# Optimization experiments

Hardware: AMD Instinct MI355X
Metric: run time of the kernel (lower is better)

Reference implementation:

```python
import jax, jax.numpy as jnp
import numpy as np

NUM_HEADS = 8
NUM_POINTS = 4


def setup_inputs() -> dict:
    key = jax.random.key(0)
    ks = jax.random.split(key, 10)
    B, H, W, D = 8, 64, 64, 256
    N = H * W
    nh, P = NUM_HEADS, NUM_POINTS

    def xavier(k, shape):
        fan_in, fan_out = shape[0], shape[1]
        lim = float(np.sqrt(6.0 / (fan_in + fan_out)))
        return jax.random.uniform(k, shape, jnp.float32, -lim, lim)

    x = jax.random.normal(ks[0], (B, N, D), jnp.float32)
    qkv_w = xavier(ks[1], (D, 3 * D))
    qkv_b = jnp.zeros((3 * D,), jnp.float32)
    # offset network is zero-init in the module; use small random weights so the
    # deformable sampling is actually exercised (offsets nonzero).
    off_w = jax.random.normal(ks[2], (D, nh * P * 2), jnp.float32) * 0.01
    off_b = jnp.zeros((nh * P * 2,), jnp.float32)
    attw_w = xavier(ks[3], (D, nh * P))
    attw_b = jnp.zeros((nh * P,), jnp.float32)
    proj_w = xavier(ks[4], (D, D))
    proj_b = jnp.zeros((D,), jnp.float32)
    return {
        "x": x, "qkv_w": qkv_w, "qkv_b": qkv_b,
        "off_w": off_w, "off_b": off_b,
        "attw_w": attw_w, "attw_b": attw_b,
        "proj_w": proj_w, "proj_b": proj_b,
        "H": 64, "W": 64,
    }


def _deformable_forward(x, qkv_w, qkv_b, off_w, off_b, attw_w, attw_b, proj_w, proj_b, H, W):
    B, N, D = x.shape
    nh, P = NUM_HEADS, NUM_POINTS
    hd = D // nh

    qkv = x @ qkv_w + qkv_b                      # [B,N,3D] (q,k computed but unused, as in the original)
    v = qkv[..., 2 * D:].reshape(B, N, nh, hd)   # [B,N,nh,hd]

    offsets = jnp.tanh((x @ off_w + off_b).reshape(B, N, nh, P, 2)) * 2.0

    ys, xs = jnp.meshgrid(jnp.arange(H, dtype=x.dtype), jnp.arange(W, dtype=x.dtype), indexing="ij")
    ref = jnp.stack([xs, ys], axis=-1).reshape(N, 2)          # [N,2] (x,y) pixel coords
    loc = ref[None, :, None, None, :] + offsets               # [B,N,nh,P,2] pixel coords
    # (module normalizes to [-1,1] then grid_sample align_corners=True un-normalizes
    #  back to exactly these pixel coordinates, so we sample at `loc` directly)

    # value as flat spatial map per head: [B,nh,hd,N], n = y*W + x
    vf = v.transpose(0, 2, 3, 1).reshape(B, nh, hd, N)

    gx, gy = loc[..., 0], loc[..., 1]
    x0 = jnp.floor(gx); y0 = jnp.floor(gy)
    x1 = x0 + 1.0;      y1 = y0 + 1.0
    wx1 = gx - x0; wx0 = 1.0 - wx1
    wy1 = gy - y0; wy0 = 1.0 - wy1

    def corner(xi, yi, w):
        # bilinear corner with zeros padding: zero weight if corner out of bounds
        valid = (xi >= 0) & (xi < W) & (yi >= 0) & (yi < H)
        idx = (jnp.clip(yi, 0, H - 1) * W + jnp.clip(xi, 0, W - 1)).astype(jnp.int32)
        idx2 = idx.transpose(0, 2, 1, 3).reshape(B, nh, N * P)          # [B,nh,N*P]
        g = jnp.take_along_axis(vf, idx2[:, :, None, :], axis=3)        # [B,nh,hd,N*P]
        w2 = (w * valid.astype(x.dtype)).transpose(0, 2, 1, 3).reshape(B, nh, 1, N * P)
        return g * w2

    sampled = (corner(x0, y0, wx0 * wy0) + corner(x1, y0, wx1 * wy0)
               + corner(x0, y1, wx0 * wy1) + corner(x1, y1, wx1 * wy1))
    sampled = sampled.reshape(B, nh, hd, N, P)

    attn = jax.nn.softmax((x @ attw_w + attw_b).reshape(B, N, nh, P), axis=-1)
    out = jnp.einsum("bhcnp,bnhp->bnhc", sampled, attn).reshape(B, N, D)
    return out @ proj_w + proj_b


def reference(x, qkv_w, qkv_b, off_w, off_b, attw_w, attw_b, proj_w, proj_b, H, W):
    return _deformable_forward(x, qkv_w, qkv_b, off_w, off_b, attw_w, attw_b, proj_w, proj_b, H, W)
```

## Files before the change

kernel.cpp:

```cpp
#include <hip/hip_runtime.h>
#include <hip/hip_bf16.h>
#include <cmath>

#define NN 4096
typedef __attribute__((ext_vector_type(8))) short short8;
typedef __attribute__((ext_vector_type(4))) float f32x4;

__device__ __forceinline__ float bf2f(unsigned short u) {
  union { unsigned int i; float f; } c; c.i = ((unsigned int)u) << 16; return c.f;
}

__global__ __launch_bounds__(256) void cvt_w(
    const float* __restrict__ qkv_w, const float* __restrict__ off_w,
    const float* __restrict__ attw_w, const float* __restrict__ proj_w,
    __hip_bfloat16* __restrict__ wcatT, __hip_bfloat16* __restrict__ pjT)
{
  const int t = threadIdx.x;
  if (blockIdx.x < 256) {
    int k = blockIdx.x;
    wcatT[t * 256 + k] = __float2bfloat16(qkv_w[k * 768 + 512 + t]);
    if (t < 128) {
      int c2 = 256 + t;
      float v = 0.f;
      if (c2 < 320)      v = off_w[k * 64 + (c2 - 256)];
      else if (c2 < 352) v = attw_w[k * 32 + (c2 - 320)];
      wcatT[c2 * 256 + k] = __float2bfloat16(v);
    }
  } else {
    int k = blockIdx.x - 256;
    pjT[t * 256 + k] = __float2bfloat16(proj_w[k * 256 + t]);
  }
}

__global__ __launch_bounds__(512) void gemm_voff(
    const float* __restrict__ x,
    const __hip_bfloat16* __restrict__ wcatT,
    const float* __restrict__ vbias,
    const float* __restrict__ off_b, const float* __restrict__ attw_b,
    __hip_bfloat16* __restrict__ vb,
    unsigned int* __restrict__ table)
{
  __shared__ float smemf[12800];
  short* As = (short*)smemf;
  short* Bs = As + 128 * 40;
  float (*L)[100] = (float(*)[100])smemf;

  const int t = threadIdx.x;
  const int m0 = blockIdx.x * 128;
  const int wave = t >> 6, lane = t & 63, q = lane >> 4, ln = lane & 15;
  const int wm = (wave & 1) * 64, wn = (wave >> 1) * 96;

  f32x4 acc[4][6] = {};

  const int arow = t >> 2, aseg = t & 3;
  const float* apg = x + (size_t)(m0 + arow) * 256 + aseg * 8;

  for (int k0 = 0; k0 < 256; k0 += 32) {
    float4 f0 = *(const float4*)(apg + k0);
    float4 f1 = *(const float4*)(apg + k0 + 4);
    alignas(16) __hip_bfloat16 cv[8] = {
      __float2bfloat16(f0.x), __float2bfloat16(f0.y), __float2bfloat16(f0.z), __float2bfloat16(f0.w),
      __float2bfloat16(f1.x), __float2bfloat16(f1.y), __float2bfloat16(f1.z), __float2bfloat16(f1.w)};
    *(int4*)&As[arow * 40 + aseg * 8] = *(int4*)cv;
#pragma unroll
    for (int i = 0; i < 3; ++i) {
      int u = t + i * 512;
      int brow = u >> 2, bseg = u & 3;
      *(int4*)&Bs[brow * 40 + bseg * 8] =
          *(const int4*)&wcatT[(size_t)brow * 256 + k0 + bseg * 8];
    }
    __syncthreads();
    short8 a[4], b[6];
#pragma unroll
    for (int i = 0; i < 4; ++i) a[i] = *(const short8*)&As[(wm + i * 16 + ln) * 40 + q * 8];
#pragma unroll
    for (int j = 0; j < 6; ++j) b[j] = *(const short8*)&Bs[(wn + j * 16 + ln) * 40 + q * 8];
#pragma unroll
    for (int i = 0; i < 4; ++i)
#pragma unroll
      for (int j = 0; j < 6; ++j)
        acc[i][j] = __builtin_amdgcn_mfma_f32_16x16x32_bf16(a[i], b[j], acc[i][j], 0, 0, 0);
    __syncthreads();
  }

#pragma unroll
  for (int j = 0; j < 6; ++j) {
    int col = wn + j * 16 + ln;
    if (col < 256) {
      float bv = vbias[col];
#pragma unroll
      for (int i = 0; i < 4; ++i) {
        int rowb = m0 + wm + i * 16 + q * 4;
#pragma unroll
        for (int r = 0; r < 4; ++r)
          vb[(size_t)(rowb + r) * 256 + col] = __float2bfloat16(acc[i][j][r] + bv);
      }
    } else if (col < 352) {
      int lc = col - 256;
      float bv = (lc < 64) ? off_b[lc] : attw_b[lc - 64];
#pragma unroll
      for (int i = 0; i < 4; ++i)
#pragma unroll
        for (int r = 0; r < 4; ++r)
          L[wm + i * 16 + q * 4 + r][lc] = acc[i][j][r] + bv;
    }
  }
  __syncthreads();

#pragma unroll
  for (int it = 0; it < 2; ++it) {
    int pl = t + it * 512;
    int rr = pl >> 3, h = pl & 7;
    int row = m0 + rr;
    int nl = row & (NN - 1);
    float refx = (float)(nl & 63);
    float refy = (float)(nl >> 6);

    float a0 = L[rr][64 + h * 4 + 0], a1 = L[rr][64 + h * 4 + 1];
    float a2 = L[rr][64 + h * 4 + 2], a3 = L[rr][64 + h * 4 + 3];
    float mx = fmaxf(fmaxf(a0, a1), fmaxf(a2, a3));
    float e0 = expf(a0 - mx), e1 = expf(a1 - mx), e2 = expf(a2 - mx), e3 = expf(a3 - mx);
    float inv = 1.f / (e0 + e1 + e2 + e3);
    float at[4] = {e0 * inv, e1 * inv, e2 * inv, e3 * inv};

    alignas(16) unsigned short idxs[16];
    alignas(16) _Float16 wsv[16];
#pragma unroll
    for (int p = 0; p < 4; ++p) {
      float gx = refx + 2.f * tanhf(L[rr][h * 8 + p * 2 + 0]);
      float gy = refy + 2.f * tanhf(L[rr][h * 8 + p * 2 + 1]);
      float x0f = floorf(gx), y0f = floorf(gy);
      int x0 = (int)x0f, y0 = (int)y0f;
      int x1 = x0 + 1,   y1 = y0 + 1;
      float wx1 = gx - x0f, wx0 = 1.f - wx1;
      float wy1 = gy - y0f, wy0 = 1.f - wy1;
      int cx0 = min(max(x0, 0), 63), cx1 = min(max(x1, 0), 63);
      int cy0 = min(max(y0, 0), 63), cy1 = min(max(y1, 0), 63);
      float vx0 = (x0 >= 0 && x0 <= 63) ? 1.f : 0.f;
      float vx1 = (x1 >= 0 && x1 <= 63) ? 1.f : 0.f;
      float vy0 = (y0 >= 0 && y0 <= 63) ? 1.f : 0.f;
      float vy1 = (y1 >= 0 && y1 <= 63) ? 1.f : 0.f;
      float ap = at[p];
      idxs[p * 4 + 0] = (unsigned short)(cy0 * 64 + cx0);
      idxs[p * 4 + 1] = (unsigned short)(cy0 * 64 + cx1);
      idxs[p * 4 + 2] = (unsigned short)(cy1 * 64 + cx0);
      idxs[p * 4 + 3] = (unsigned short)(cy1 * 64 + cx1);
      wsv[p * 4 + 0] = (_Float16)(ap * wx0 * wy0 * vx0 * vy0);
      wsv[p * 4 + 1] = (_Float16)(ap * wx1 * wy0 * vx1 * vy0);
      wsv[p * 4 + 2] = (_Float16)(ap * wx0 * wy1 * vx0 * vy1);
      wsv[p * 4 + 3] = (_Float16)(ap * wx1 * wy1 * vx1 * vy1);
    }
    uint4* dst = (uint4*)(table + ((size_t)row * 8 + h) * 16);
    dst[0] = *(uint4*)&idxs[0];
    dst[1] = *(uint4*)&idxs[8];
    dst[2] = *(uint4*)&wsv[0];
    dst[3] = *(uint4*)&wsv[8];
  }
}

__global__ __launch_bounds__(256) void sample_kernel(
    const __hip_bfloat16* __restrict__ v,
    const unsigned int* __restrict__ table,
    __hip_bfloat16* __restrict__ y)
{
  __shared__ uint4 Tab[256];
  const int t = threadIdx.x;
  const int p0 = blockIdx.x * 64;
  Tab[t] = *(const uint4*)(table + (size_t)p0 * 16 + t * 4);
  __syncthreads();

  const int g = t & 3, p = t >> 2;
  const int pg = p0 + p;
  const int h = pg & 7;
  const int row = pg >> 3;
  const int b = row >> 12;
  const unsigned short* ip = (const unsigned short*)&Tab[p * 4];
  const _Float16* wp = (const _Float16*)((const char*)&Tab[p * 4] + 32);
  const char* vbase = (const char*)(v + (size_t)b * NN * 256 + h * 32 + g * 8);

  float acc[8] = {};
#pragma unroll
  for (int j = 0; j < 16; ++j) {
    float w = (float)wp[j];
    int idx = ip[j];
    int4 pk = *(const int4*)(vbase + (size_t)idx * 512);
    const unsigned short* u = (const unsigned short*)&pk;
#pragma unroll
    for (int c = 0; c < 8; ++c) acc[c] += w * bf2f(u[c]);
  }
  alignas(16) __hip_bfloat16 o[8];
#pragma unroll
  for (int c = 0; c < 8; ++c) o[c] = __float2bfloat16(acc[c]);
  *(int4*)((char*)y + ((size_t)row * 256 + h * 32 + g * 8) * 2) = *(int4*)o;
}

__global__ __launch_bounds__(256) void gemm_proj(
    const short* __restrict__ A, const short* __restrict__ BT,
    const float* __restrict__ bias, float* __restrict__ out)
{
  __shared__ short As[128 * 40];
  __shared__ short Bs[128 * 40];
  const int t = threadIdx.x;
  const int m0 = blockIdx.y * 128, n0 = blockIdx.x * 128;
  const int wave = t >> 6, lane = t & 63, q = lane >> 4, ln = lane & 15;
  const int wm = (wave & 1) * 64, wn = (wave >> 1) * 64;

  f32x4 acc[4][4] = {};

  for (int k0 = 0; k0 < 256; k0 += 32) {
#pragma unroll
    for (int u = 0; u < 2; ++u) {
      int c = t + u * 256;
      int row = c >> 2, kq = c & 3;
      *(int4*)&As[row * 40 + kq * 8] =
          *(const int4*)&A[(size_t)(m0 + row) * 256 + k0 + kq * 8];
      *(int4*)&Bs[row * 40 + kq * 8] =
          *(const int4*)&BT[(size_t)(n0 + row) * 256 + k0 + kq * 8];
    }
    __syncthreads();
    short8 a[4], b[4];
#pragma unroll
    for (int i = 0; i < 4; ++i) a[i] = *(const short8*)&As[(wm + i * 16 + ln) * 40 + q * 8];
#pragma unroll
    for (int j = 0; j < 4; ++j) b[j] = *(const short8*)&Bs[(wn + j * 16 + ln) * 40 + q * 8];
#pragma unroll
    for (int i = 0; i < 4; ++i)
#pragma unroll
      for (int j = 0; j < 4; ++j)
        acc[i][j] = __builtin_amdgcn_mfma_f32_16x16x32_bf16(a[i], b[j], acc[i][j], 0, 0, 0);
    __syncthreads();
  }

#pragma unroll
  for (int j = 0; j < 4; ++j) {
    int col = n0 + wn + j * 16 + ln;
    float bv = bias[col];
#pragma unroll
    for (int i = 0; i < 4; ++i) {
      int rowb = m0 + wm + i * 16 + q * 4;
#pragma unroll
      for (int r = 0; r < 4; ++r)
        out[(size_t)(rowb + r) * 256 + col] = acc[i][j][r] + bv;
    }
  }
}

extern "C" void kernel_launch(void* const* d_in, const int* in_sizes, int n_in,
                              void* d_out, int out_size, void* d_ws, size_t ws_size,
                              hipStream_t stream) {
  const float* x      = (const float*)d_in[0];
  const float* qkv_w  = (const float*)d_in[1];
  const float* qkv_b  = (const float*)d_in[2];
  const float* off_w  = (const float*)d_in[3];
  const float* off_b  = (const float*)d_in[4];
  const float* attw_w = (const float*)d_in[5];
  const float* attw_b = (const float*)d_in[6];
  const float* proj_w = (const float*)d_in[7];
  const float* proj_b = (const float*)d_in[8];
  float* out = (float*)d_out;

  char* ws = (char*)d_ws;
  __hip_bfloat16* vb    = (__hip_bfloat16*)(ws);
  __hip_bfloat16* yb    = (__hip_bfloat16*)(ws + 16777216);
  unsigned int*   table = (unsigned int*)  (ws + 33554432);
  __hip_bfloat16* wcatT = (__hip_bfloat16*)(ws + 50331648);
  __hip_bfloat16* pjT   = (__hip_bfloat16*)(ws + 50528256);

  cvt_w<<<512, 256, 0, stream>>>(qkv_w, off_w, attw_w, proj_w, wcatT, pjT);
  gemm_voff<<<256, 512, 0, stream>>>(x, wcatT, qkv_b + 512, off_b, attw_b, vb, table);
  sample_kernel<<<4096, 256, 0, stream>>>(vb, table, yb);
  dim3 g2(2, 256);
  gemm_proj<<<g2, 256, 0, stream>>>((const short*)yb, (const short*)pjT, proj_b, out);
}
```

Measured before the change: 152.6 us.

## Fuse deformable sampling into projection GEMM and shrink voff GEMM tiles

The bilinear sampling kernel and the output projection GEMM become one kernel. Each 64-row block gathers its sampled values into an LDS tile and multiplies it by the projection weights there. This removes the intermediate y buffer write/read and one launch. The value/offset GEMM also moves to 64-row tiles with 256 threads, giving 512 blocks instead of 256. The costs are that the projection weights are reloaded for every 64-row block, and the larger LDS footprint may reduce occupancy while the gather phase runs.

After: 169.8 us. 1.11x slower.

```diff
diff --git a/kernel.cpp b/kernel.cpp
--- a/kernel.cpp
+++ b/kernel.cpp
@@ -32,7 +32,7 @@
   }
 }
 
-__global__ __launch_bounds__(512) void gemm_voff(
+__global__ __launch_bounds__(256) void gemm_voff(
     const float* __restrict__ x,
     const __hip_bfloat16* __restrict__ wcatT,
     const float* __restrict__ vbias,
@@ -40,15 +40,15 @@
     __hip_bfloat16* __restrict__ vb,
     unsigned int* __restrict__ table)
 {
-  __shared__ float smemf[12800];
+  __shared__ float smemf[8960];
   short* As = (short*)smemf;
-  short* Bs = As + 128 * 40;
+  short* Bs = As + 64 * 40;
   float (*L)[100] = (float(*)[100])smemf;
 
   const int t = threadIdx.x;
-  const int m0 = blockIdx.x * 128;
+  const int m0 = blockIdx.x * 64;
   const int wave = t >> 6, lane = t & 63, q = lane >> 4, ln = lane & 15;
-  const int wm = (wave & 1) * 64, wn = (wave >> 1) * 96;
+  const int wn = wave * 96;
 
   f32x4 acc[4][6] = {};
 
@@ -63,8 +63,8 @@
       __float2bfloat16(f1.x), __float2bfloat16(f1.y), __float2bfloat16(f1.z), __float2bfloat16(f1.w)};
     *(int4*)&As[arow * 40 + aseg * 8] = *(int4*)cv;
 #pragma unroll
-    for (int i = 0; i < 3; ++i) {
-      int u = t + i * 512;
+    for (int i = 0; i < 6; ++i) {
+      int u = t + i * 256;
       int brow = u >> 2, bseg = u & 3;
       *(int4*)&Bs[brow * 40 + bseg * 8] =
           *(const int4*)&wcatT[(size_t)brow * 256 + k0 + bseg * 8];
@@ -72,7 +72,7 @@
     __syncthreads();
     short8 a[4], b[6];
 #pragma unroll
-    for (int i = 0; i < 4; ++i) a[i] = *(const short8*)&As[(wm + i * 16 + ln) * 40 + q * 8];
+    for (int i = 0; i < 4; ++i) a[i] = *(const short8*)&As[(i * 16 + ln) * 40 + q * 8];
 #pragma unroll
     for (int j = 0; j < 6; ++j) b[j] = *(const short8*)&Bs[(wn + j * 16 + ln) * 40 + q * 8];
 #pragma unroll
@@ -90,7 +90,7 @@
       float bv = vbias[col];
 #pragma unroll
       for (int i = 0; i < 4; ++i) {
-        int rowb = m0 + wm + i * 16 + q * 4;
+        int rowb = m0 + i * 16 + q * 4;
 #pragma unroll
         for (int r = 0; r < 4; ++r)
           vb[(size_t)(rowb + r) * 256 + col] = __float2bfloat16(acc[i][j][r] + bv);
@@ -102,14 +102,14 @@
       for (int i = 0; i < 4; ++i)
 #pragma unroll
         for (int r = 0; r < 4; ++r)
-          L[wm + i * 16 + q * 4 + r][lc] = acc[i][j][r] + bv;
+          L[i * 16 + q * 4 + r][lc] = acc[i][j][r] + bv;
     }
   }
   __syncthreads();
 
 #pragma unroll
   for (int it = 0; it < 2; ++it) {
-    int pl = t + it * 512;
+    int pl = t + it * 256;
     int rr = pl >> 3, h = pl & 7;
     int row = m0 + rr;
     int nl = row & (NN - 1);
@@ -158,86 +158,80 @@
   }
 }
 
-__global__ __launch_bounds__(256) void sample_kernel(
-    const __hip_bfloat16* __restrict__ v,
+__global__ __launch_bounds__(256) void gemm_sproj(
+    const __hip_bfloat16* __restrict__ vb,
     const unsigned int* __restrict__ table,
-    __hip_bfloat16* __restrict__ y)
+    const __hip_bfloat16* __restrict__ pjT,
+    const float* __restrict__ bias,
+    float* __restrict__ out)
 {
-  __shared__ uint4 Tab[256];
+  __shared__ short ytile[64 * 264];
+  __shared__ short Bs[256 * 40];
   const int t = threadIdx.x;
-  const int p0 = blockIdx.x * 64;
-  Tab[t] = *(const uint4*)(table + (size_t)p0 * 16 + t * 4);
+  const int m0 = blockIdx.x * 64;
+  const int wave = t >> 6, lane = t & 63, q = lane >> 4, ln = lane & 15;
+  const int wn = wave * 64;
+  const int b = m0 >> 12;
+
+#pragma unroll
+  for (int i = 0; i < 8; ++i) {
+    int tau = t + i * 256;
+    int r = tau >> 5, h = (tau >> 2) & 7, g = tau & 3;
+    int row = m0 + r;
+    const uint4* tp = (const uint4*)(table + ((size_t)row * 8 + h) * 16);
+    uint4 e0 = tp[0], e1 = tp[1];
+    uint4 e2 = tp[2], e3 = tp[3];
+    const unsigned int iw[8] = {e0.x, e0.y, e0.z, e0.w, e1.x, e1.y, e1.z, e1.w};
+    const unsigned int ww[8] = {e2.x, e2.y, e2.z, e2.w, e3.x, e3.y, e3.z, e3.w};
+    const char* vbase = (const char*)(vb + ((size_t)b * NN * 256) + h * 32 + g * 8);
+    float accg[8] = {};
+#pragma unroll
+    for (int j = 0; j < 16; ++j) {
+      unsigned int idx = (iw[j >> 1] >> ((j & 1) * 16)) & 0xffffu;
+      union { unsigned int u; _Float16 h2[2]; } wu; wu.u = ww[j >> 1];
+      float w = (float)wu.h2[j & 1];
+      int4 pk = *(const int4*)(vbase + (size_t)idx * 512);
+      const unsigned short* uu = (const unsigned short*)&pk;
+#pragma unroll
+      for (int c = 0; c < 8; ++c) accg[c] += w * bf2f(uu[c]);
+    }
+    alignas(16) __hip_bfloat16 o[8];
+#pragma unroll
+    for (int c = 0; c < 8; ++c) o[c] = __float2bfloat16(accg[c]);
+    *(int4*)&ytile[r * 264 + h * 32 + g * 8] = *(int4*)o;
+  }
   __syncthreads();
 
-  const int g = t & 3, p = t >> 2;
-  const int pg = p0 + p;
-  const int h = pg & 7;
-  const int row = pg >> 3;
-  const int b = row >> 12;
-  const unsigned short* ip = (const unsigned short*)&Tab[p * 4];
-  const _Float16* wp = (const _Float16*)((const char*)&Tab[p * 4] + 32);
-  const char* vbase = (const char*)(v + (size_t)b * NN * 256 + h * 32 + g * 8);
-
-  float acc[8] = {};
-#pragma unroll
-  for (int j = 0; j < 16; ++j) {
-    float w = (float)wp[j];
-    int idx = ip[j];
-    int4 pk = *(const int4*)(vbase + (size_t)idx * 512);
-    const unsigned short* u = (const unsigned short*)&pk;
-#pragma unroll
-    for (int c = 0; c < 8; ++c) acc[c] += w * bf2f(u[c]);
-  }
-  alignas(16) __hip_bfloat16 o[8];
-#pragma unroll
-  for (int c = 0; c < 8; ++c) o[c] = __float2bfloat16(acc[c]);
-  *(int4*)((char*)y + ((size_t)row * 256 + h * 32 + g * 8) * 2) = *(int4*)o;
-}
-
-__global__ __launch_bounds__(256) void gemm_proj(
-    const short* __restrict__ A, const short* __restrict__ BT,
-    const float* __restrict__ bias, float* __restrict__ out)
-{
-  __shared__ short As[128 * 40];
-  __shared__ short Bs[128 * 40];
-  const int t = threadIdx.x;
-  const int m0 = blockIdx.y * 128, n0 = blockIdx.x * 128;
-  const int wave = t >> 6, lane = t & 63, q = lane >> 4, ln = lane & 15;
-  const int wm = (wave & 1) * 64, wn = (wave >> 1) * 64;
-
   f32x4 acc[4][4] = {};
-
   for (int k0 = 0; k0 < 256; k0 += 32) {
 #pragma unroll
-    for (int u = 0; u < 2; ++u) {
-      int c = t + u * 256;
-      int row = c >> 2, kq = c & 3;
-      *(int4*)&As[row * 40 + kq * 8] =
-          *(const int4*)&A[(size_t)(m0 + row) * 256 + k0 + kq * 8];
-      *(int4*)&Bs[row * 40 + kq * 8] =
-          *(const int4*)&BT[(size_t)(n0 + row) * 256 + k0 + kq * 8];
-    }
-    __syncthreads();
-    short8 a[4], b[4];
-#pragma unroll
-    for (int i = 0; i < 4; ++i) a[i] = *(const short8*)&As[(wm + i * 16 + ln) * 40 + q * 8];
-#pragma unroll
-    for (int j = 0; j < 4; ++j) b[j] = *(const short8*)&Bs[(wn + j * 16 + ln) * 40 + q * 8];
+    for (int i = 0; i < 4; ++i) {
+      int u = t + i * 256;
+      int brow = u >> 2, bseg = u & 3;
+      *(int4*)&Bs[brow * 40 + bseg * 8] =
+          *(const int4*)&pjT[(size_t)brow * 256 + k0 + bseg * 8];
+    }
+    __syncthreads();
+    short8 a[4], bfr[4];
+#pragma unroll
+    for (int i = 0; i < 4; ++i) a[i] = *(const short8*)&ytile[(i * 16 + ln) * 264 + k0 + q * 8];
+#pragma unroll
+    for (int j = 0; j < 4; ++j) bfr[j] = *(const short8*)&Bs[(wn + j * 16 + ln) * 40 + q * 8];
 #pragma unroll
     for (int i = 0; i < 4; ++i)
 #pragma unroll
       for (int j = 0; j < 4; ++j)
-        acc[i][j] = __builtin_amdgcn_mfma_f32_16x16x32_bf16(a[i], b[j], acc[i][j], 0, 0, 0);
+        acc[i][j] = __builtin_amdgcn_mfma_f32_16x16x32_bf16(a[i], bfr[j], acc[i][j], 0, 0, 0);
     __syncthreads();
   }
 
 #pragma unroll
   for (int j = 0; j < 4; ++j) {
-    int col = n0 + wn + j * 16 + ln;
+    int col = wn + j * 16 + ln;
     float bv = bias[col];
 #pragma unroll
     for (int i = 0; i < 4; ++i) {
-      int rowb = m0 + wm + i * 16 + q * 4;
+      int rowb = m0 + i * 16 + q * 4;
 #pragma unroll
       for (int r = 0; r < 4; ++r)
         out[(size_t)(rowb + r) * 256 + col] = acc[i][j][r] + bv;
@@ -261,14 +255,11 @@
 
   char* ws = (char*)d_ws;
   __hip_bfloat16* vb    = (__hip_bfloat16*)(ws);
-  __hip_bfloat16* yb    = (__hip_bfloat16*)(ws + 16777216);
-  unsigned int*   table = (unsigned int*)  (ws + 33554432);
-  __hip_bfloat16* wcatT = (__hip_bfloat16*)(ws + 50331648);
-  __hip_bfloat16* pjT   = (__hip_bfloat16*)(ws + 50528256);
+  unsigned int*   table = (unsigned int*)  (ws + 16777216);
+  __hip_bfloat16* wcatT = (__hip_bfloat16*)(ws + 33554432);
+  __hip_bfloat16* pjT   = (__hip_bfloat16*)(ws + 33751040);
 
   cvt_w<<<512, 256, 0, stream>>>(qkv_w, off_w, attw_w, proj_w, wcatT, pjT);
-  gemm_voff<<<256, 512, 0, stream>>>(x, wcatT, qkv_b + 512, off_b, attw_b, vb, table);
-  sample_kernel<<<4096, 256, 0, stream>>>(vb, table, yb);
-  dim3 g2(2, 256);
-  gemm_proj<<<g2, 256, 0, stream>>>((const short*)yb, (const short*)pjT, proj_b, out);
-}
+  gemm_voff<<<512, 256, 0, stream>>>(x, wcatT, qkv_b + 512, off_b, attw_b, vb, table);
+  gemm_sproj<<<512, 256, 0, stream>>>(vb, table, pjT, proj_b, out);
+}
```
